# Kernel optimization log

Hardware: AMD Instinct MI355X
Metric: run time of the kernel (lower is better)

## Reference

```python
import jax, jax.numpy as jnp
import numpy as np

DIM = 1024
HEADS = 16
HEAD_DIM = DIM // HEADS
HIDDEN = 4096
EPS = 1e-5


def _layer_norm(x, w, b):
    mu = jnp.mean(x, axis=-1, keepdims=True)
    var = jnp.var(x, axis=-1, keepdims=True)
    return (x - mu) * jax.lax.rsqrt(var + EPS) * w + b


def setup_inputs() -> dict:
    key = jax.random.key(0)
    ks = jax.random.split(key, 16)
    s = lambda fan_in: 1.0 / np.sqrt(fan_in)
    return {
        "x": jax.random.normal(ks[0], (8, 1024, DIM), dtype=jnp.float32),
        "ln1_w": jnp.ones((DIM,), jnp.float32),
        "ln1_b": jnp.zeros((DIM,), jnp.float32),
        "qkv_w": jax.random.uniform(ks[1], (3 * DIM, DIM), jnp.float32, -s(DIM), s(DIM)),
        "qkv_b": jax.random.uniform(ks[2], (3 * DIM,), jnp.float32, -s(DIM), s(DIM)),
        "out_w": jax.random.uniform(ks[3], (DIM, DIM), jnp.float32, -s(DIM), s(DIM)),
        "out_b": jax.random.uniform(ks[4], (DIM,), jnp.float32, -s(DIM), s(DIM)),
        "ln2_w": jnp.ones((DIM,), jnp.float32),
        "ln2_b": jnp.zeros((DIM,), jnp.float32),
        "fc1_w": jax.random.uniform(ks[5], (HIDDEN, DIM), jnp.float32, -s(DIM), s(DIM)),
        "fc1_b": jax.random.uniform(ks[6], (HIDDEN,), jnp.float32, -s(DIM), s(DIM)),
        "fc2_w": jax.random.uniform(ks[7], (DIM, HIDDEN), jnp.float32, -s(HIDDEN), s(HIDDEN)),
        "fc2_b": jax.random.uniform(ks[8], (DIM,), jnp.float32, -s(HIDDEN), s(HIDDEN)),
    }


def reference(x, ln1_w, ln1_b, qkv_w, qkv_b, out_w, out_b,
              ln2_w, ln2_b, fc1_w, fc1_b, fc2_w, fc2_b):
    B, S, D = x.shape
    # --- attention sub-block (pre-LN) ---
    h = _layer_norm(x, ln1_w, ln1_b)
    qkv = h @ qkv_w.T + qkv_b                              # [B,S,3D]
    qkv = qkv.reshape(B, S, 3, HEADS, HEAD_DIM)
    q, k, v = qkv[:, :, 0], qkv[:, :, 1], qkv[:, :, 2]     # [B,S,H,hd]
    scores = jnp.einsum('bqhd,bkhd->bhqk', q, k) / np.sqrt(HEAD_DIM)
    attn = jax.nn.softmax(scores, axis=-1)
    o = jnp.einsum('bhqk,bkhd->bqhd', attn, v).reshape(B, S, D)
    x = x + (o @ out_w.T + out_b)
    # --- MLP sub-block (pre-LN) ---
    h = _layer_norm(x, ln2_w, ln2_b)
    h = jax.nn.gelu(h @ fc1_w.T + fc1_b, approximate=False)
    x = x + (h @ fc2_w.T + fc2_b)
    return x
```

## Files before the change

### kernel.cpp

```cpp
#include <hip/hip_runtime.h>
#include <hip/hip_bf16.h>

typedef unsigned short u16;
typedef __bf16 bf16x8 __attribute__((ext_vector_type(8)));
typedef float f32x4 __attribute__((ext_vector_type(4)));
typedef u16 u16x8 __attribute__((ext_vector_type(8)));
typedef unsigned u32x2 __attribute__((ext_vector_type(2)));

#define LOG2E 1.4426950408889634f
#define QSCALE 0.18033688011112042f

__device__ __forceinline__ float fast_exp2(float x) {
#if __has_builtin(__builtin_amdgcn_exp2f)
  return __builtin_amdgcn_exp2f(x);
#else
  return exp2f(x);
#endif
}

__device__ __forceinline__ u16 f2bf(float f) {
  union { float f; unsigned u; } c; c.f = f;
  unsigned r = c.u + 0x7fffu + ((c.u >> 16) & 1u);
  return (u16)(r >> 16);
}

__device__ __forceinline__ unsigned pk_bf16(float a, float b) {
#if __has_builtin(__builtin_amdgcn_cvt_pk_bf16_f32)
  typedef __bf16 bf16x2_t __attribute__((ext_vector_type(2)));
  union { bf16x2_t v; unsigned u; } c;
  c.v = __builtin_amdgcn_cvt_pk_bf16_f32(a, b);
  return c.u;
#else
  return (unsigned)f2bf(a) | ((unsigned)f2bf(b) << 16);
#endif
}

__device__ __forceinline__ unsigned pk_bf16_fast(float a, float b) {
#if __has_builtin(__builtin_amdgcn_cvt_pk_bf16_f32)
  return pk_bf16(a, b);
#else
  union { float f; unsigned u; } ca, cb;
  ca.f = a; cb.f = b;
  return __builtin_amdgcn_perm(cb.u, ca.u, 0x07060302u);
#endif
}

__device__ __forceinline__ float gelu_f(float v) {
  float z = 0.7978845608f * v + 0.0356774081f * (v * v * v);
  float e = fast_exp2(z * 2.885390082f);
  float t = 1.0f - 2.0f * __builtin_amdgcn_rcpf(e + 1.0f);
  return 0.5f * v * (1.0f + t);
}

__device__ __forceinline__ void async16(const void* g, void* l) {
  __builtin_amdgcn_global_load_lds(
      (const __attribute__((address_space(1))) void*)g,
      (__attribute__((address_space(3))) void*)l, 16, 0, 0);
}

__global__ __launch_bounds__(256) void cvt4_kernel(
    const float* __restrict__ s0, const float* __restrict__ s1,
    const float* __restrict__ s2, const float* __restrict__ s3,
    u16* __restrict__ d0, u16* __restrict__ d1,
    u16* __restrict__ d2, u16* __restrict__ d3) {
  int i = blockIdx.x * 256 + threadIdx.x;
  const float* s; u16* d; int off;
  if (i < 786432)       { s = s0; d = d0; off = i; }
  else if (i < 1048576) { s = s1; d = d1; off = i - 786432; }
  else if (i < 2097152) { s = s2; d = d2; off = i - 1048576; }
  else                  { s = s3; d = d3; off = i - 2097152; }
  float4 v = ((const float4*)s)[off];
  ushort4 o;
  o.x = f2bf(v.x); o.y = f2bf(v.y); o.z = f2bf(v.z); o.w = f2bf(v.w);
  ((ushort4*)d)[off] = o;
}

__global__ __launch_bounds__(256) void ln_kernel(const float* __restrict__ x,
                                                 const float* __restrict__ w,
                                                 const float* __restrict__ b,
                                                 u16* __restrict__ out) {
  int row = blockIdx.x;
  int tid = threadIdx.x;
  int lane = tid & 63, wave = tid >> 6;
  float4 v = ((const float4*)(x + (size_t)row * 1024))[tid];
  float s = v.x + v.y + v.z + v.w;
  float s2 = v.x*v.x + v.y*v.y + v.z*v.z + v.w*v.w;
  #pragma unroll
  for (int off = 1; off < 64; off <<= 1) {
    s += __shfl_xor(s, off, 64);
    s2 += __shfl_xor(s2, off, 64);
  }
  __shared__ float red[8];
  if (lane == 0) { red[wave] = s; red[4 + wave] = s2; }
  __syncthreads();
  float st = red[0] + red[1] + red[2] + red[3];
  float s2t = red[4] + red[5] + red[6] + red[7];
  float mu = st * (1.0f / 1024.0f);
  float var = s2t * (1.0f / 1024.0f) - mu * mu;
  float rs = rsqrtf(var + 1e-5f);
  float4 wv = ((const float4*)w)[tid];
  float4 bv = ((const float4*)b)[tid];
  ushort4 o;
  o.x = f2bf((v.x - mu) * rs * wv.x + bv.x);
  o.y = f2bf((v.y - mu) * rs * wv.y + bv.y);
  o.z = f2bf((v.z - mu) * rs * wv.z + bv.z);
  o.w = f2bf((v.w - mu) * rs * wv.w + bv.w);
  ((ushort4*)(out + (size_t)row * 1024))[tid] = o;
}

template <int EPI, int TN>
__global__ __launch_bounds__(256) void gemm_bt(const u16* __restrict__ A,
                                               const u16* __restrict__ B,
                                               const float* __restrict__ bias,
                                               void* __restrict__ Cout,
                                               const float* __restrict__ resid,
                                               int M, int N, int K) {
  constexpr int NT = TN / 32;
  __shared__ u16 As[128 * 64];
  __shared__ u16 Bs[TN * 64];
  const int tid = threadIdx.x;
  const int lane = tid & 63, wave = tid >> 6;
  const int l15 = lane & 15, l4 = lane >> 4;
  const int m0 = blockIdx.y * 128, n0 = blockIdx.x * TN;
  const int wr = (wave & 1) * 64, wc = (wave >> 1) * (TN / 2);

  const int srow = lane >> 3;
  const int sg = (lane & 7) ^ (lane >> 3);
  const size_t K8 = (size_t)8 * K;
  const u16* Ag = A + (size_t)(m0 + wave * 32 + srow) * K + sg * 8;
  const u16* Bg = B + (size_t)(n0 + wave * (TN / 4) + srow) * K + sg * 8;
  u16* Al0 = As + wave * 2048;
  u16* Bl0 = Bs + wave * (TN / 4) * 64;
  const int rx = l15 & 7;

  f32x4 acc[4][NT];
  #pragma unroll
  for (int i = 0; i < 4; i++)
    #pragma unroll
    for (int j = 0; j < NT; j++) {
      f32x4 z = {0.f, 0.f, 0.f, 0.f};
      acc[i][j] = z;
    }

  for (int k0 = 0; k0 < K; k0 += 64) {
    __syncthreads();
    #pragma unroll
    for (int t = 0; t < 4; t++) async16(Ag + t * K8 + k0, Al0 + t * 512);
    #pragma unroll
    for (int t = 0; t < NT; t++) async16(Bg + t * K8 + k0, Bl0 + t * 512);
    __syncthreads();
    #pragma unroll
    for (int ks = 0; ks < 2; ks++) {
      const int pg = ((ks * 4 + l4) ^ rx) * 8;
      bf16x8 a[4], b[NT];
      #pragma unroll
      for (int rg = 0; rg < 4; rg++)
        a[rg] = *(const bf16x8*)&As[(wr + rg * 16 + l15) * 64 + pg];
      #pragma unroll
      for (int tg = 0; tg < NT; tg++)
        b[tg] = *(const bf16x8*)&Bs[(wc + tg * 16 + l15) * 64 + pg];
      #pragma unroll
      for (int rg = 0; rg < 4; rg++)
        #pragma unroll
        for (int tg = 0; tg < NT; tg++)
          acc[rg][tg] = __builtin_amdgcn_mfma_f32_16x16x32_bf16(
              a[rg], b[tg], acc[rg][tg], 0, 0, 0);
    }
  }

  float bv[NT];
  #pragma unroll
  for (int tg = 0; tg < NT; tg++) bv[tg] = bias[n0 + wc + tg * 16 + l15];
  #pragma unroll
  for (int rg = 0; rg < 4; rg++) {
    size_t row0 = (size_t)(m0 + wr + rg * 16 + l4 * 4);
    #pragma unroll
    for (int r = 0; r < 4; r += 2) {
      #pragma unroll
      for (int tg = 0; tg < NT; tg++) {
        int col = n0 + wc + tg * 16 + l15;
        float v0 = acc[rg][tg][r] + bv[tg];
        float v1 = acc[rg][tg][r + 1] + bv[tg];
        if (EPI == 1) { v0 = gelu_f(v0); v1 = gelu_f(v1); }
        if (EPI == 3) {
          float sc = (col < 1024) ? QSCALE : 1.0f;
          v0 *= sc; v1 *= sc;
        }
        size_t off0 = (row0 + r) * (size_t)N + col;
        size_t off1 = (row0 + r + 1) * (size_t)N + col;
        if (EPI == 2) {
          ((float*)Cout)[off0] = v0 + resid[off0];
          ((float*)Cout)[off1] = v1 + resid[off1];
        } else {
          unsigned pk = pk_bf16(v0, v1);
          ((u16*)Cout)[off0] = (u16)pk;
          ((u16*)Cout)[off1] = (u16)(pk >> 16);
        }
      }
    }
  }
}

__global__ __launch_bounds__(256) void vtrans_kernel(const u16* __restrict__ qkv,
                                                     u16* __restrict__ vtg) {
  const int sc = blockIdx.x, h = blockIdx.y, b = blockIdx.z;
  const int tid = threadIdx.x;
  __shared__ u16 t[64][72];
  const u16* vp = qkv + ((size_t)b * 1024) * 3072 + h * 64 + 2048;
  #pragma unroll
  for (int it = 0; it < 2; it++) {
    int idx = it * 256 + tid;
    int row = idx >> 3, g = idx & 7;
    *(u16x8*)&t[row][g * 8] =
        *(const u16x8*)(vp + (size_t)(sc * 64 + row) * 3072 + g * 8);
  }
  __syncthreads();
  u16* dst = vtg + ((size_t)(b * 16 + h) * 64) * 1024;
  #pragma unroll
  for (int it = 0; it < 2; it++) {
    int idx = it * 256 + tid;
    int d = idx >> 3, g = idx & 7;
    u16x8 o;
    #pragma unroll
    for (int j = 0; j < 8; j++) o[j] = t[g * 8 + j][d];
    *(u16x8*)(dst + (size_t)d * 1024 + sc * 64 + g * 8) = o;
  }
}

__global__ __launch_bounds__(256) void attn_kernel(const u16* __restrict__ qkv,
                                                   const u16* __restrict__ vtg,
                                                   u16* __restrict__ obuf) {
  const int S = 1024, QKV = 3072;
  const int id = blockIdx.x;
  const int qt = id >> 7, hb = id & 127;
  const int h = hb & 15, b = hb >> 4;
  const int tid = threadIdx.x, lane = tid & 63, wave = tid >> 6;
  const int l15 = lane & 15, l4 = lane >> 4;
  const size_t tok0 = (size_t)b * S;
  const u16* qp = qkv + tok0 * QKV + h * 64;
  const u16* kp = qp + 1024;
  const u16* vtp = vtg + (size_t)(b * 16 + h) * 64 * 1024;
  const int q0 = qt * 64;

  __shared__ u16 Ks[128 * 64];
  __shared__ u16 Vt[64 * 128];
  __shared__ u16 Ps[4][16 * 136];

  const u16* qrow = qp + (size_t)(q0 + wave * 16 + l15) * QKV;
  bf16x8 qf[2];
  #pragma unroll
  for (int kb = 0; kb < 2; kb++)
    qf[kb] = *(const bf16x8*)(qrow + kb * 32 + l4 * 8);

  bf16x8 ones;
  #pragma unroll
  for (int j = 0; j < 8; j++) ones[j] = (__bf16)1.0f;

  const int krow = lane >> 3;
  const int klg = (lane & 7) ^ (lane >> 3);
  const int vrow_i = lane >> 4;
  const int vpg = lane & 15;

  f32x4 oacc[4], lacc;
  #pragma unroll
  for (int ct = 0; ct < 4; ct++) {
    f32x4 z = {0.f, 0.f, 0.f, 0.f};
    oacc[ct] = z;
  }
  { f32x4 z = {0.f, 0.f, 0.f, 0.f}; lacc = z; }

  for (int j0 = 0; j0 < S; j0 += 128) {
    __syncthreads();
    #pragma unroll
    for (int t = 0; t < 4; t++) {
      int e = wave * 4 + t;
      async16(kp + (size_t)(j0 + e * 8 + krow) * QKV + klg * 8, Ks + e * 512);
    }
    #pragma unroll
    for (int t = 0; t < 4; t++) {
      int e = wave * 4 + t;
      int row = e * 4 + vrow_i;
      int lg = vpg ^ (row & 15);
      async16(vtp + (size_t)row * 1024 + j0 + lg * 8, Vt + e * 512);
    }
    __syncthreads();

    f32x4 s[8];
    #pragma unroll
    for (int tg = 0; tg < 8; tg++) {
      f32x4 z = {0.f, 0.f, 0.f, 0.f};
      s[tg] = z;
      #pragma unroll
      for (int kb = 0; kb < 2; kb++) {
        int pg = (kb * 4 + l4) ^ (l15 & 7);
        bf16x8 kf = *(const bf16x8*)&Ks[(tg * 16 + l15) * 64 + pg * 8];
        s[tg] = __builtin_amdgcn_mfma_f32_16x16x32_bf16(kf, qf[kb], s[tg], 0, 0, 0);
      }
    }

    #pragma unroll
    for (int tg = 0; tg < 8; tg++)
      #pragma unroll
      for (int r = 0; r < 4; r++)
        s[tg][r] = fast_exp2(s[tg][r]);

    #pragma unroll
    for (int tg = 0; tg < 8; tg++) {
      u32x2 pr;
      pr[0] = pk_bf16_fast(s[tg][0], s[tg][1]);
      pr[1] = pk_bf16_fast(s[tg][2], s[tg][3]);
      *(u32x2*)&Ps[wave][l15 * 136 + tg * 16 + l4 * 4] = pr;
    }
    bf16x8 pf[4];
    #pragma unroll
    for (int kb = 0; kb < 4; kb++)
      pf[kb] = *(const bf16x8*)&Ps[wave][l15 * 136 + kb * 32 + l4 * 8];

    #pragma unroll
    for (int kb = 0; kb < 4; kb++) {
      #pragma unroll
      for (int ct = 0; ct < 4; ct++) {
        int pg = (kb * 4 + l4) ^ l15;
        bf16x8 vf = *(const bf16x8*)&Vt[(ct * 16 + l15) * 128 + pg * 8];
        oacc[ct] = __builtin_amdgcn_mfma_f32_16x16x32_bf16(pf[kb], vf, oacc[ct], 0, 0, 0);
      }
      lacc = __builtin_amdgcn_mfma_f32_16x16x32_bf16(pf[kb], ones, lacc, 0, 0, 0);
    }
  }

  float inv[4];
  #pragma unroll
  for (int r = 0; r < 4; r++) inv[r] = 1.0f / lacc[r];
  #pragma unroll
  for (int ct = 0; ct < 4; ct++)
    #pragma unroll
    for (int r = 0; r < 4; r++) {
      float v = oacc[ct][r] * inv[r];
      size_t row = tok0 + q0 + wave * 16 + l4 * 4 + r;
      obuf[row * 1024 + h * 64 + ct * 16 + l15] = f2bf(v);
    }
}

extern "C" void kernel_launch(void* const* d_in, const int* in_sizes, int n_in,
                              void* d_out, int out_size, void* d_ws, size_t ws_size,
                              hipStream_t stream) {
  (void)in_sizes; (void)n_in; (void)out_size; (void)ws_size;
  const float* x     = (const float*)d_in[0];
  const float* ln1_w = (const float*)d_in[1];
  const float* ln1_b = (const float*)d_in[2];
  const float* qkv_w = (const float*)d_in[3];
  const float* qkv_b = (const float*)d_in[4];
  const float* out_w = (const float*)d_in[5];
  const float* out_b = (const float*)d_in[6];
  const float* ln2_w = (const float*)d_in[7];
  const float* ln2_b = (const float*)d_in[8];
  const float* fc1_w = (const float*)d_in[9];
  const float* fc1_b = (const float*)d_in[10];
  const float* fc2_w = (const float*)d_in[11];
  const float* fc2_b = (const float*)d_in[12];
  float* out = (float*)d_out;

  char* ws = (char*)d_ws;
  u16* wqkv = (u16*)(ws);
  u16* wout = (u16*)(ws + 6291456);
  u16* wfc1 = (u16*)(ws + 8388608);
  u16* wfc2 = (u16*)(ws + 16777216);
  u16* hbuf = (u16*)(ws + 25165824);
  u16* qbuf = (u16*)(ws + 41943040);
  u16* vtg  = (u16*)(ws + 92274688);

  const int M = 8192;

  cvt4_kernel<<<dim3(12288), 256, 0, stream>>>(qkv_w, out_w, fc1_w, fc2_w,
                                               wqkv, wout, wfc1, wfc2);

  ln_kernel<<<dim3(M), 256, 0, stream>>>(x, ln1_w, ln1_b, hbuf);
  gemm_bt<3, 128><<<dim3(3072 / 128, M / 128), 256, 0, stream>>>(
      hbuf, wqkv, qkv_b, qbuf, nullptr, M, 3072, 1024);
  vtrans_kernel<<<dim3(16, 16, 8), 256, 0, stream>>>(qbuf, vtg);
  attn_kernel<<<dim3(2048), 256, 0, stream>>>(qbuf, vtg, hbuf);
  gemm_bt<2, 64><<<dim3(1024 / 64, M / 128), 256, 0, stream>>>(
      hbuf, wout, out_b, out, x, M, 1024, 1024);
  ln_kernel<<<dim3(M), 256, 0, stream>>>(out, ln2_w, ln2_b, hbuf);
  gemm_bt<1, 128><<<dim3(4096 / 128, M / 128), 256, 0, stream>>>(
      hbuf, wfc1, fc1_b, qbuf, nullptr, M, 4096, 1024);
  gemm_bt<2, 64><<<dim3(1024 / 64, M / 128), 256, 0, stream>>>(
      qbuf, wfc2, fc2_b, out, out, M, 1024, 4096);
}
```

Baseline: 484.9 us.

## Process two query tiles per attention block and remap fc2 GEMM blocks per XCD

The attention kernel now handles 128 queries per block (two 64-row sub-tiles per wave), so each K/V tile loaded into shared memory is reused twice and the grid halves. The fc2 GEMM switches to a 1D grid that assigns consecutive M-tiles to the same XCD (id&7) and walks all N-tiles of an M-row within that XCD, aiming to improve L2 reuse of the A rows. Costs are more registers per attention wave and fewer blocks (1024) for occupancy.

```diff
diff --git a/kernel.cpp b/kernel.cpp
--- a/kernel.cpp
+++ b/kernel.cpp
@@ -108,7 +108,7 @@
   ((ushort4*)(out + (size_t)row * 1024))[tid] = o;
 }
 
-template <int EPI, int TN>
+template <int EPI, int TN, int NBLOG2>
 __global__ __launch_bounds__(256) void gemm_bt(const u16* __restrict__ A,
                                                const u16* __restrict__ B,
                                                const float* __restrict__ bias,
@@ -121,7 +121,19 @@
   const int tid = threadIdx.x;
   const int lane = tid & 63, wave = tid >> 6;
   const int l15 = lane & 15, l4 = lane >> 4;
-  const int m0 = blockIdx.y * 128, n0 = blockIdx.x * TN;
+
+  int m0, n0;
+  if (NBLOG2 < 0) {
+    m0 = blockIdx.y * 128; n0 = blockIdx.x * TN;
+  } else {
+    const int id = blockIdx.x;
+    const int xcd = id & 7;
+    const int slot = id >> 3;
+    const int ms = slot >> (NBLOG2 < 0 ? 0 : NBLOG2);
+    const int nt = slot & ((1 << (NBLOG2 < 0 ? 0 : NBLOG2)) - 1);
+    m0 = (ms * 8 + xcd) * 128; n0 = nt * TN;
+  }
+
   const int wr = (wave & 1) * 64, wc = (wave >> 1) * (TN / 2);
 
   const int srow = lane >> 3;
@@ -240,17 +252,19 @@
   const u16* qp = qkv + tok0 * QKV + h * 64;
   const u16* kp = qp + 1024;
   const u16* vtp = vtg + (size_t)(b * 16 + h) * 64 * 1024;
-  const int q0 = qt * 64;
+  const int q0 = qt * 128;
 
   __shared__ u16 Ks[128 * 64];
   __shared__ u16 Vt[64 * 128];
   __shared__ u16 Ps[4][16 * 136];
 
   const u16* qrow = qp + (size_t)(q0 + wave * 16 + l15) * QKV;
-  bf16x8 qf[2];
-  #pragma unroll
-  for (int kb = 0; kb < 2; kb++)
-    qf[kb] = *(const bf16x8*)(qrow + kb * 32 + l4 * 8);
+  bf16x8 qf[2][2];
+  #pragma unroll
+  for (int qs = 0; qs < 2; qs++)
+    #pragma unroll
+    for (int kb = 0; kb < 2; kb++)
+      qf[qs][kb] = *(const bf16x8*)(qrow + (size_t)qs * 64 * QKV + kb * 32 + l4 * 8);
 
   bf16x8 ones;
   #pragma unroll
@@ -261,13 +275,17 @@
   const int vrow_i = lane >> 4;
   const int vpg = lane & 15;
 
-  f32x4 oacc[4], lacc;
-  #pragma unroll
-  for (int ct = 0; ct < 4; ct++) {
+  f32x4 oacc[2][4], lacc[2];
+  #pragma unroll
+  for (int qs = 0; qs < 2; qs++) {
+    #pragma unroll
+    for (int ct = 0; ct < 4; ct++) {
+      f32x4 z = {0.f, 0.f, 0.f, 0.f};
+      oacc[qs][ct] = z;
+    }
     f32x4 z = {0.f, 0.f, 0.f, 0.f};
-    oacc[ct] = z;
-  }
-  { f32x4 z = {0.f, 0.f, 0.f, 0.f}; lacc = z; }
+    lacc[qs] = z;
+  }
 
   for (int j0 = 0; j0 < S; j0 += 128) {
     __syncthreads();
@@ -285,60 +303,68 @@
     }
     __syncthreads();
 
-    f32x4 s[8];
-    #pragma unroll
-    for (int tg = 0; tg < 8; tg++) {
-      f32x4 z = {0.f, 0.f, 0.f, 0.f};
-      s[tg] = z;
-      #pragma unroll
-      for (int kb = 0; kb < 2; kb++) {
-        int pg = (kb * 4 + l4) ^ (l15 & 7);
-        bf16x8 kf = *(const bf16x8*)&Ks[(tg * 16 + l15) * 64 + pg * 8];
-        s[tg] = __builtin_amdgcn_mfma_f32_16x16x32_bf16(kf, qf[kb], s[tg], 0, 0, 0);
+    #pragma unroll
+    for (int qs = 0; qs < 2; qs++) {
+      f32x4 s[8];
+      #pragma unroll
+      for (int tg = 0; tg < 8; tg++) {
+        f32x4 z = {0.f, 0.f, 0.f, 0.f};
+        s[tg] = z;
+        #pragma unroll
+        for (int kb = 0; kb < 2; kb++) {
+          int pg = (kb * 4 + l4) ^ (l15 & 7);
+          bf16x8 kf = *(const bf16x8*)&Ks[(tg * 16 + l15) * 64 + pg * 8];
+          s[tg] = __builtin_amdgcn_mfma_f32_16x16x32_bf16(kf, qf[qs][kb], s[tg], 0, 0, 0);
+        }
       }
-    }
-
-    #pragma unroll
-    for (int tg = 0; tg < 8; tg++)
-      #pragma unroll
-      for (int r = 0; r < 4; r++)
-        s[tg][r] = fast_exp2(s[tg][r]);
-
-    #pragma unroll
-    for (int tg = 0; tg < 8; tg++) {
-      u32x2 pr;
-      pr[0] = pk_bf16_fast(s[tg][0], s[tg][1]);
-      pr[1] = pk_bf16_fast(s[tg][2], s[tg][3]);
-      *(u32x2*)&Ps[wave][l15 * 136 + tg * 16 + l4 * 4] = pr;
-    }
-    bf16x8 pf[4];
-    #pragma unroll
-    for (int kb = 0; kb < 4; kb++)
-      pf[kb] = *(const bf16x8*)&Ps[wave][l15 * 136 + kb * 32 + l4 * 8];
-
-    #pragma unroll
-    for (int kb = 0; kb < 4; kb++) {
-      #pragma unroll
-      for (int ct = 0; ct < 4; ct++) {
-        int pg = (kb * 4 + l4) ^ l15;
-        bf16x8 vf = *(const bf16x8*)&Vt[(ct * 16 + l15) * 128 + pg * 8];
-        oacc[ct] = __builtin_amdgcn_mfma_f32_16x16x32_bf16(pf[kb], vf, oacc[ct], 0, 0, 0);
+
+      #pragma unroll
+      for (int tg = 0; tg < 8; tg++)
+        #pragma unroll
+        for (int r = 0; r < 4; r++)
+          s[tg][r] = fast_exp2(s[tg][r]);
+
+      #pragma unroll
+      for (int tg = 0; tg < 8; tg++) {
+        u32x2 pr;
+        pr[0] = pk_bf16_fast(s[tg][0], s[tg][1]);
+        pr[1] = pk_bf16_fast(s[tg][2], s[tg][3]);
+        *(u32x2*)&Ps[wave][l15 * 136 + tg * 16 + l4 * 4] = pr;
       }
-      lacc = __builtin_amdgcn_mfma_f32_16x16x32_bf16(pf[kb], ones, lacc, 0, 0, 0);
-    }
-  }
-
-  float inv[4];
-  #pragma unroll
-  for (int r = 0; r < 4; r++) inv[r] = 1.0f / lacc[r];
-  #pragma unroll
-  for (int ct = 0; ct < 4; ct++)
-    #pragma unroll
-    for (int r = 0; r < 4; r++) {
-      float v = oacc[ct][r] * inv[r];
-      size_t row = tok0 + q0 + wave * 16 + l4 * 4 + r;
-      obuf[row * 1024 + h * 64 + ct * 16 + l15] = f2bf(v);
-    }
+      bf16x8 pf[4];
+      #pragma unroll
+      for (int kb = 0; kb < 4; kb++)
+        pf[kb] = *(const bf16x8*)&Ps[wave][l15 * 136 + kb * 32 + l4 * 8];
+
+      #pragma unroll
+      for (int kb = 0; kb < 4; kb++) {
+        #pragma unroll
+        for (int ct = 0; ct < 4; ct++) {
+          int pg = (kb * 4 + l4) ^ l15;
+          bf16x8 vf = *(const bf16x8*)&Vt[(ct * 16 + l15) * 128 + pg * 8];
+          oacc[qs][ct] = __builtin_amdgcn_mfma_f32_16x16x32_bf16(
+              pf[kb], vf, oacc[qs][ct], 0, 0, 0);
+        }
+        lacc[qs] = __builtin_amdgcn_mfma_f32_16x16x32_bf16(
+            pf[kb], ones, lacc[qs], 0, 0, 0);
+      }
+    }
+  }
+
+  #pragma unroll
+  for (int qs = 0; qs < 2; qs++) {
+    float inv[4];
+    #pragma unroll
+    for (int r = 0; r < 4; r++) inv[r] = 1.0f / lacc[qs][r];
+    #pragma unroll
+    for (int ct = 0; ct < 4; ct++)
+      #pragma unroll
+      for (int r = 0; r < 4; r++) {
+        float v = oacc[qs][ct][r] * inv[r];
+        size_t row = tok0 + q0 + qs * 64 + wave * 16 + l4 * 4 + r;
+        obuf[row * 1024 + h * 64 + ct * 16 + l15] = f2bf(v);
+      }
+  }
 }
 
 extern "C" void kernel_launch(void* const* d_in, const int* in_sizes, int n_in,
@@ -375,15 +401,15 @@
                                                wqkv, wout, wfc1, wfc2);
 
   ln_kernel<<<dim3(M), 256, 0, stream>>>(x, ln1_w, ln1_b, hbuf);
-  gemm_bt<3, 128><<<dim3(3072 / 128, M / 128), 256, 0, stream>>>(
+  gemm_bt<3, 128, -1><<<dim3(3072 / 128, M / 128), 256, 0, stream>>>(
       hbuf, wqkv, qkv_b, qbuf, nullptr, M, 3072, 1024);
   vtrans_kernel<<<dim3(16, 16, 8), 256, 0, stream>>>(qbuf, vtg);
-  attn_kernel<<<dim3(2048), 256, 0, stream>>>(qbuf, vtg, hbuf);
-  gemm_bt<2, 64><<<dim3(1024 / 64, M / 128), 256, 0, stream>>>(
+  attn_kernel<<<dim3(1024), 256, 0, stream>>>(qbuf, vtg, hbuf);
+  gemm_bt<2, 64, -1><<<dim3(1024 / 64, M / 128), 256, 0, stream>>>(
       hbuf, wout, out_b, out, x, M, 1024, 1024);
   ln_kernel<<<dim3(M), 256, 0, stream>>>(out, ln2_w, ln2_b, hbuf);
-  gemm_bt<1, 128><<<dim3(4096 / 128, M / 128), 256, 0, stream>>>(
+  gemm_bt<1, 128, -1><<<dim3(4096 / 128, M / 128), 256, 0, stream>>>(
       hbuf, wfc1, fc1_b, qbuf, nullptr, M, 4096, 1024);
-  gemm_bt<2, 64><<<dim3(1024 / 64, M / 128), 256, 0, stream>>>(
+  gemm_bt<2, 64, 4><<<dim3((M / 128) * 16), 256, 0, stream>>>(
       qbuf, wfc2, fc2_b, out, out, M, 1024, 4096);
 }
```

Result: no change. 479.8 us (-1.0%).
